# Optimization experiments

Hardware: AMD Instinct MI355X
Metric: run time of the kernel (lower is better)

Reference implementation:

```python
import jax, jax.numpy as jnp
import numpy as np

X_DIM = 512
Y_DIM = 512
HID = 300
N = 2048


def setup_inputs() -> dict:
    key = jax.random.key(0)
    ks = jax.random.split(key, 8)
    scale = 0.05
    return {
        "pos_local": jax.random.normal(ks[0], (N, X_DIM), jnp.float32),
        "pos_global": jax.random.normal(ks[1], (N, Y_DIM), jnp.float32),
        "neg_local": jax.random.normal(ks[2], (N, X_DIM), jnp.float32),
        "neg_global": jax.random.normal(ks[3], (N, Y_DIM), jnp.float32),
        "W1": jax.random.normal(ks[4], (X_DIM + Y_DIM, HID), jnp.float32) * scale,
        "b1": jnp.zeros((HID,), jnp.float32),
        "W2": jax.random.normal(ks[5], (HID, 1), jnp.float32) * scale,
        "b2": jnp.zeros((1,), jnp.float32),
        "batch_size": 256,
    }


def reference(pos_local, pos_global, neg_local, neg_global, W1, b1, W2, b2, batch_size):
    # Split first-layer weight into local/global halves so we never materialize
    # the concatenated pair tensor: F(cat(l, g)) uses l @ W1l + g @ W1g.
    W1l, W1g = W1[:X_DIM], W1[X_DIM:]
    w2, bias2 = W2[:, 0], b2[0]

    # Positive branch: plain batched MLP, chunking does not change the math.
    h0 = jax.nn.relu(pos_local @ W1l + pos_global @ W1g + b1)  # [N, HID]
    t0 = jax.nn.softplus(h0 @ w2 + bias2).mean()

    # Negative branch: per chunk of size B, pair (local_j, global_i),
    # score[i, j] = F(local_j, global_i); logsumexp over j, mean over i.
    nc = neg_local.shape[0] // batch_size
    nl = neg_local.reshape(nc, batch_size, X_DIM)
    ng = neg_global.reshape(nc, batch_size, Y_DIM)

    def chunk_term(carry, lg):
        l, g = lg                                   # [B, x], [B, y]
        lp = l @ W1l                                # [B, HID]
        gp = g @ W1g                                # [B, HID]
        h = jax.nn.relu(gp[:, None, :] + lp[None, :, :] + b1)  # [B, B, HID]
        s = jax.nn.softplus(h @ w2 + bias2)         # [B, B]
        val = jax.scipy.special.logsumexp(s, axis=1).mean()
        return carry + val, None

    total, _ = jax.lax.scan(chunk_term, jnp.float32(0.0), (nl, ng))
    t1 = total / nc

    lower_bound = t0 - t1
    return -lower_bound
```

## Files before the change

kernel.cpp:

```cpp
#include <hip/hip_runtime.h>
#include <math.h>

#define NR   2048
#define XD   512
#define HID  300
#define BS   256
#define NPAD 320
#define KTOT 1024
#define GSTR 304
#define KP   320
#define NNEG 256

typedef __attribute__((ext_vector_type(8))) short bf16x8;
typedef __attribute__((ext_vector_type(4))) float f32x4;

__device__ __forceinline__ float softplus_f(float x) {
    return fmaxf(x, 0.f) + log1pf(__expf(-fabsf(x)));
}
__device__ __forceinline__ unsigned short f2bf(float f) {
    unsigned int u = __float_as_uint(f);
    u += 0x7FFFu + ((u >> 16) & 1u);
    return (unsigned short)(u >> 16);
}

__global__ __launch_bounds__(256) void convert(
    const float* __restrict__ pl, const float* __restrict__ pg,
    const float* __restrict__ nl, const float* __restrict__ ng,
    const float* __restrict__ W1,
    unsigned short* __restrict__ Aneg, unsigned short* __restrict__ Apos,
    unsigned short* __restrict__ Wt, unsigned int* __restrict__ counter)
{
    const int b = blockIdx.x, tid = threadIdx.x;
    if (b == 0 && tid == 0) *counter = 0u;
    if (b < 4096) {
        const int m = (b < 2048) ? b : b - 2048;
        const float* lo = (b < 2048) ? nl : pl;
        const float* hi = (b < 2048) ? ng : pg;
        unsigned short* dst = (b < 2048) ? Aneg : Apos;
        const int kq = tid * 4;
        const float4 v = (kq < XD) ? *(const float4*)(lo + m * XD + kq)
                                   : *(const float4*)(hi + m * XD + kq - XD);
        ushort4 o;
        o.x = f2bf(v.x); o.y = f2bf(v.y); o.z = f2bf(v.z); o.w = f2bf(v.w);
        *(ushort4*)(dst + m * KTOT + kq) = o;
    } else {
        __shared__ unsigned short ts[16][72];
        const int t = b - 4096;
        const int nt = t % 20, kt = t / 20;
        const int n = nt * 16 + (tid & 15);
        const int kl = tid >> 4;
        #pragma unroll
        for (int j = 0; j < 4; ++j) {
            const int k = kt * 64 + kl * 4 + j;
            ts[tid & 15][kl * 4 + j] = f2bf((n < HID) ? W1[k * HID + n] : 0.f);
        }
        __syncthreads();
        const int nw = tid >> 4, kw = (tid & 15) * 4;
        ushort4 o;
        o.x = ts[nw][kw]; o.y = ts[nw][kw + 1]; o.z = ts[nw][kw + 2]; o.w = ts[nw][kw + 3];
        *(ushort4*)(Wt + (nt * 16 + nw) * KTOT + kt * 64 + kw) = o;
    }
}

__global__ __launch_bounds__(64) void mfma_gemm(
    const unsigned short* __restrict__ Aneg, const unsigned short* __restrict__ Apos,
    const unsigned short* __restrict__ Wt, const float* __restrict__ b1,
    float* __restrict__ LP4, float* __restrict__ GPB,
    float* __restrict__ P0a, float* __restrict__ P0b)
{
    const int job = blockIdx.z;
    const int m0 = blockIdx.x * 32, n0 = blockIdx.y * 32;
    const int lane = threadIdx.x;
    const int r = lane & 15, g = lane >> 4;

    const unsigned short* A = (job >= 2) ? Apos : Aneg;
    const int kbeg = (job & 1) ? XD : 0;

    const unsigned short* a0p = A  + (m0 + r) * KTOT + kbeg + 8 * g;
    const unsigned short* a1p = a0p + 16 * KTOT;
    const unsigned short* b0p = Wt + (n0 + r) * KTOT + kbeg + 8 * g;
    const unsigned short* b1p = b0p + 16 * KTOT;

    f32x4 acc00 = {0,0,0,0}, acc01 = {0,0,0,0}, acc10 = {0,0,0,0}, acc11 = {0,0,0,0};

    #pragma unroll
    for (int k = 0; k < XD; k += 32) {
        const bf16x8 a0 = *(const bf16x8*)(a0p + k);
        const bf16x8 a1 = *(const bf16x8*)(a1p + k);
        const bf16x8 w0 = *(const bf16x8*)(b0p + k);
        const bf16x8 w1 = *(const bf16x8*)(b1p + k);
        acc00 = __builtin_amdgcn_mfma_f32_16x16x32_bf16(a0, w0, acc00, 0, 0, 0);
        acc01 = __builtin_amdgcn_mfma_f32_16x16x32_bf16(a0, w1, acc01, 0, 0, 0);
        acc10 = __builtin_amdgcn_mfma_f32_16x16x32_bf16(a1, w0, acc10, 0, 0, 0);
        acc11 = __builtin_amdgcn_mfma_f32_16x16x32_bf16(a1, w1, acc11, 0, 0, 0);
    }

    f32x4 accs[2][2] = {{acc00, acc01}, {acc10, acc11}};
    #pragma unroll
    for (int mi = 0; mi < 2; ++mi) {
        #pragma unroll
        for (int ni = 0; ni < 2; ++ni) {
            const int n = n0 + ni * 16 + r;
            const int mb = m0 + mi * 16 + 4 * g;
            const f32x4 v = accs[mi][ni];
            if (job == 0) {
                float* base = LP4 + ((size_t)(n >> 2) * NR + mb) * 4 + (n & 3);
                base[0] = v[0]; base[4] = v[1]; base[8] = v[2]; base[12] = v[3];
            } else if (n < HID) {
                const float bias = (job == 1) ? b1[n] : 0.f;
                float* out = (job == 1) ? GPB : ((job == 2) ? P0a : P0b);
                #pragma unroll
                for (int j = 0; j < 4; ++j)
                    out[(size_t)(mb + j) * GSTR + n] = v[j] + bias;
            }
        }
    }
}

__global__ __launch_bounds__(512, 2) void negpos(
    const float* __restrict__ LP4, const float* __restrict__ GPB,
    const float* __restrict__ P0a, const float* __restrict__ P0b,
    const float* __restrict__ b1, const float* __restrict__ W2,
    const float* __restrict__ b2,
    float* __restrict__ negE, float* __restrict__ posP,
    unsigned int* __restrict__ counter, float* __restrict__ out)
{
    __shared__ __align__(16) float w2s[KP];
    __shared__ __align__(16) float gbs[8][KP];
    __shared__ __align__(16) float pacc[8][BS][8];
    __shared__ float sC[8];
    __shared__ float red[4][8];
    __shared__ float redp[8];
    __shared__ int sh_last;
    const int tid = threadIdx.x, bid = blockIdx.x;
    const int kh = tid >> 6, lh = tid & 63;
    const float b2v = b2[0];

    const int chunk = bid >> 5, g0 = (bid & 31) * 8;
    const float* gp = GPB + (size_t)(chunk * BS + g0) * GSTR;
    for (int idx = tid; idx < KP; idx += 512) {
        const bool v = idx < HID;
        w2s[idx] = v ? 0.5f * W2[idx] : 0.f;
        #pragma unroll
        for (int g = 0; g < 8; ++g)
            gbs[g][idx] = v ? gp[g * GSTR + idx] : 0.f;
    }
    __syncthreads();

    {
        float c = 0.f;
        #pragma unroll
        for (int h = 0; h < 2; ++h) {
            const int k4 = lh + 64 * h;
            if (k4 < 80) {
                const float4 g4 = *(const float4*)&gbs[kh][k4 * 4];
                const float4 w4 = *(const float4*)&w2s[k4 * 4];
                c += g4.x * w4.x + g4.y * w4.y + g4.z * w4.z + g4.w * w4.w;
            }
        }
        #pragma unroll
        for (int o = 32; o > 0; o >>= 1) c += __shfl_xor(c, o);
        if (lh == 0) sC[kh] = c;
    }

    const int k4beg = 10 * kh;
    const float4* lpb = (const float4*)LP4 + (chunk * BS + lh);

    float acc[8][4];
    float q[4] = {0.f, 0.f, 0.f, 0.f};
    #pragma unroll
    for (int gt = 0; gt < 8; ++gt)
        #pragma unroll
        for (int j = 0; j < 4; ++j) acc[gt][j] = 0.f;

    #pragma unroll
    for (int i = 0; i < 10; ++i) {
        const int k4 = k4beg + i;
        float4 a[4];
        #pragma unroll
        for (int j = 0; j < 4; ++j)
            a[j] = lpb[(size_t)k4 * NR + 64 * j];
        const float4 w4 = *(const float4*)&w2s[k4 * 4];
        #pragma unroll
        for (int j = 0; j < 4; ++j) {
            q[j] = fmaf(w4.x, a[j].x, q[j]);
            q[j] = fmaf(w4.y, a[j].y, q[j]);
            q[j] = fmaf(w4.z, a[j].z, q[j]);
            q[j] = fmaf(w4.w, a[j].w, q[j]);
        }
        #pragma unroll
        for (int gt = 0; gt < 8; ++gt) {
            const float4 g4 = *(const float4*)&gbs[gt][k4 * 4];
            #pragma unroll
            for (int j = 0; j < 4; ++j) {
                acc[gt][j] = fmaf(fabsf(g4.x + a[j].x), w4.x, acc[gt][j]);
                acc[gt][j] = fmaf(fabsf(g4.y + a[j].y), w4.y, acc[gt][j]);
                acc[gt][j] = fmaf(fabsf(g4.z + a[j].z), w4.z, acc[gt][j]);
                acc[gt][j] = fmaf(fabsf(g4.w + a[j].w), w4.w, acc[gt][j]);
            }
        }
    }

    #pragma unroll
    for (int j = 0; j < 4; ++j) {
        *(float4*)&pacc[kh][lh + 64 * j][0] =
            make_float4(acc[0][j] + q[j], acc[1][j] + q[j],
                        acc[2][j] + q[j], acc[3][j] + q[j]);
        *(float4*)&pacc[kh][lh + 64 * j][4] =
            make_float4(acc[4][j] + q[j], acc[5][j] + q[j],
                        acc[6][j] + q[j], acc[7][j] + q[j]);
    }
    __syncthreads();

    if (tid < 256) {
        float s[8];
        #pragma unroll
        for (int gt = 0; gt < 8; ++gt) s[gt] = sC[gt];
        #pragma unroll
        for (int k = 0; k < 8; ++k) {
            const float4 p0 = *(const float4*)&pacc[k][tid][0];
            const float4 p1 = *(const float4*)&pacc[k][tid][4];
            s[0] += p0.x; s[1] += p0.y; s[2] += p0.z; s[3] += p0.w;
            s[4] += p1.x; s[5] += p1.y; s[6] += p1.z; s[7] += p1.w;
        }
        const int wid = tid >> 6;
        #pragma unroll
        for (int gt = 0; gt < 8; ++gt) {
            float v = __expf(softplus_f(s[gt] + b2v));
            #pragma unroll
            for (int o = 32; o > 0; o >>= 1) v += __shfl_xor(v, o);
            if ((tid & 63) == 0) red[wid][gt] = v;
        }
    }
    __syncthreads();
    if (tid == 0) {
        #pragma unroll
        for (int gt = 0; gt < 8; ++gt)
            negE[bid * 8 + gt] = red[0][gt] + red[1][gt] + red[2][gt] + red[3][gt];
    }

    {
        const int row = bid * 8 + kh;
        const float4* ra = (const float4*)(P0a + (size_t)row * GSTR);
        const float4* rb = (const float4*)(P0b + (size_t)row * GSTR);
        float d = 0.f;
        #pragma unroll
        for (int h = 0; h < 2; ++h) {
            const int k4 = lh + 64 * h;
            if (k4 < 75) {
                const float4 aa = ra[k4], bb4 = rb[k4];
                const float4 bb = *(const float4*)(b1 + k4 * 4);
                const float4 wv = *(const float4*)(W2 + k4 * 4);
                d += fmaxf(aa.x + bb4.x + bb.x, 0.f) * wv.x
                   + fmaxf(aa.y + bb4.y + bb.y, 0.f) * wv.y
                   + fmaxf(aa.z + bb4.z + bb.z, 0.f) * wv.z
                   + fmaxf(aa.w + bb4.w + bb.w, 0.f) * wv.w;
            }
        }
        #pragma unroll
        for (int o = 32; o > 0; o >>= 1) d += __shfl_xor(d, o);
        if (lh == 0) redp[kh] = softplus_f(d + b2v);
    }
    __syncthreads();

    if (tid == 0) {
        posP[bid] = redp[0] + redp[1] + redp[2] + redp[3]
                  + redp[4] + redp[5] + redp[6] + redp[7];
        __threadfence();
        const unsigned t = atomicAdd(counter, 1u);
        sh_last = (t == NNEG - 1) ? 1 : 0;
    }
    __syncthreads();
    if (sh_last) {
        __threadfence();
        const volatile float* ne = (const volatile float*)negE;
        const volatile float* pp = (const volatile float*)posP;
        float v = 0.f;
        for (int i = tid; i < 2048; i += 512)
            v += __logf(ne[i]);
        if (tid < NNEG) v -= pp[tid];
        #pragma unroll
        for (int o = 32; o > 0; o >>= 1) v += __shfl_xor(v, o);
        if (lh == 0) redp[kh] = v;
        __syncthreads();
        if (tid == 0)
            out[0] = (redp[0] + redp[1] + redp[2] + redp[3]
                    + redp[4] + redp[5] + redp[6] + redp[7]) * (1.f / 2048.f);
    }
}

extern "C" void kernel_launch(void* const* d_in, const int* in_sizes, int n_in,
                              void* d_out, int out_size, void* d_ws, size_t ws_size,
                              hipStream_t stream)
{
    const float* pl = (const float*)d_in[0];
    const float* pg = (const float*)d_in[1];
    const float* nl = (const float*)d_in[2];
    const float* ng = (const float*)d_in[3];
    const float* W1 = (const float*)d_in[4];
    const float* b1 = (const float*)d_in[5];
    const float* W2 = (const float*)d_in[6];
    const float* b2 = (const float*)d_in[7];

    char* ws = (char*)d_ws;
    unsigned short* Aneg = (unsigned short*)(ws);
    unsigned short* Apos = (unsigned short*)(ws + (4u << 20));
    unsigned short* Wt   = (unsigned short*)(ws + (8u << 20));
    float* LP4  = (float*)(ws + (9u << 20));
    float* GPB  = (float*)(ws + (12u << 20));
    float* P0a  = (float*)(ws + (15u << 20));
    float* P0b  = (float*)(ws + (18u << 20));
    float* negE = (float*)(ws + (21u << 20));
    float* posP = negE + 2048;
    unsigned int* counter = (unsigned int*)(ws + (21u << 20) + 65536);
    float* out  = (float*)d_out;

    hipLaunchKernelGGL(convert, dim3(4096 + 320), dim3(256), 0, stream,
                       pl, pg, nl, ng, W1, Aneg, Apos, Wt, counter);
    hipLaunchKernelGGL(mfma_gemm, dim3(NR / 32, NPAD / 32, 4), dim3(64), 0, stream,
                       Aneg, Apos, Wt, b1, LP4, GPB, P0a, P0b);
    hipLaunchKernelGGL(negpos, dim3(NNEG), dim3(512), 0, stream,
                       LP4, GPB, P0a, P0b, b1, W2, b2, negE, posP, counter, out);
}
```

Measured before the change: 62.31 us.

## Fuse activation bf16 conversion into GEMM and widen negpos blocks to 1024 threads

The standalone conversion of the four activation matrices to bf16 is removed. The GEMM now reads fp32 activations directly and converts them in registers, so the bf16 staging buffers are neither written nor re-read. Only W1 is still pre-converted by a smaller kernel. The pairwise negpos kernel goes from 512 to 1024 threads, splitting the hidden dimension across 16 waves, and runs the positive-branch dot products in parallel with the per-global constant. In exchange it uses twice the shared partial buffer and a launch_bounds(1024,4) register limit that may cause spills, and GEMM tiles re-read fp32 activations at double the byte width.

```diff
diff --git a/kernel.cpp b/kernel.cpp
--- a/kernel.cpp
+++ b/kernel.cpp
@@ -22,48 +22,40 @@
     u += 0x7FFFu + ((u >> 16) & 1u);
     return (unsigned short)(u >> 16);
 }
-
-__global__ __launch_bounds__(256) void convert(
+__device__ __forceinline__ bf16x8 cvt8(const float4 f0, const float4 f1) {
+    bf16x8 r;
+    r[0] = (short)f2bf(f0.x); r[1] = (short)f2bf(f0.y);
+    r[2] = (short)f2bf(f0.z); r[3] = (short)f2bf(f0.w);
+    r[4] = (short)f2bf(f1.x); r[5] = (short)f2bf(f1.y);
+    r[6] = (short)f2bf(f1.z); r[7] = (short)f2bf(f1.w);
+    return r;
+}
+
+__global__ __launch_bounds__(256) void wconvert(
+    const float* __restrict__ W1, unsigned short* __restrict__ Wt,
+    unsigned int* __restrict__ counter)
+{
+    __shared__ unsigned short ts[16][72];
+    const int t = blockIdx.x, tid = threadIdx.x;
+    if (t == 0 && tid == 0) *counter = 0u;
+    const int nt = t % 20, kt = t / 20;
+    const int n = nt * 16 + (tid & 15);
+    const int kl = tid >> 4;
+    #pragma unroll
+    for (int j = 0; j < 4; ++j) {
+        const int k = kt * 64 + kl * 4 + j;
+        ts[tid & 15][kl * 4 + j] = f2bf((n < HID) ? W1[k * HID + n] : 0.f);
+    }
+    __syncthreads();
+    const int nw = tid >> 4, kw = (tid & 15) * 4;
+    ushort4 o;
+    o.x = ts[nw][kw]; o.y = ts[nw][kw + 1]; o.z = ts[nw][kw + 2]; o.w = ts[nw][kw + 3];
+    *(ushort4*)(Wt + (nt * 16 + nw) * KTOT + kt * 64 + kw) = o;
+}
+
+__global__ __launch_bounds__(64) void mfma_gemm(
+    const float* __restrict__ nl, const float* __restrict__ ng,
     const float* __restrict__ pl, const float* __restrict__ pg,
-    const float* __restrict__ nl, const float* __restrict__ ng,
-    const float* __restrict__ W1,
-    unsigned short* __restrict__ Aneg, unsigned short* __restrict__ Apos,
-    unsigned short* __restrict__ Wt, unsigned int* __restrict__ counter)
-{
-    const int b = blockIdx.x, tid = threadIdx.x;
-    if (b == 0 && tid == 0) *counter = 0u;
-    if (b < 4096) {
-        const int m = (b < 2048) ? b : b - 2048;
-        const float* lo = (b < 2048) ? nl : pl;
-        const float* hi = (b < 2048) ? ng : pg;
-        unsigned short* dst = (b < 2048) ? Aneg : Apos;
-        const int kq = tid * 4;
-        const float4 v = (kq < XD) ? *(const float4*)(lo + m * XD + kq)
-                                   : *(const float4*)(hi + m * XD + kq - XD);
-        ushort4 o;
-        o.x = f2bf(v.x); o.y = f2bf(v.y); o.z = f2bf(v.z); o.w = f2bf(v.w);
-        *(ushort4*)(dst + m * KTOT + kq) = o;
-    } else {
-        __shared__ unsigned short ts[16][72];
-        const int t = b - 4096;
-        const int nt = t % 20, kt = t / 20;
-        const int n = nt * 16 + (tid & 15);
-        const int kl = tid >> 4;
-        #pragma unroll
-        for (int j = 0; j < 4; ++j) {
-            const int k = kt * 64 + kl * 4 + j;
-            ts[tid & 15][kl * 4 + j] = f2bf((n < HID) ? W1[k * HID + n] : 0.f);
-        }
-        __syncthreads();
-        const int nw = tid >> 4, kw = (tid & 15) * 4;
-        ushort4 o;
-        o.x = ts[nw][kw]; o.y = ts[nw][kw + 1]; o.z = ts[nw][kw + 2]; o.w = ts[nw][kw + 3];
-        *(ushort4*)(Wt + (nt * 16 + nw) * KTOT + kt * 64 + kw) = o;
-    }
-}
-
-__global__ __launch_bounds__(64) void mfma_gemm(
-    const unsigned short* __restrict__ Aneg, const unsigned short* __restrict__ Apos,
     const unsigned short* __restrict__ Wt, const float* __restrict__ b1,
     float* __restrict__ LP4, float* __restrict__ GPB,
     float* __restrict__ P0a, float* __restrict__ P0b)
@@ -73,20 +65,20 @@
     const int lane = threadIdx.x;
     const int r = lane & 15, g = lane >> 4;
 
-    const unsigned short* A = (job >= 2) ? Apos : Aneg;
-    const int kbeg = (job & 1) ? XD : 0;
-
-    const unsigned short* a0p = A  + (m0 + r) * KTOT + kbeg + 8 * g;
-    const unsigned short* a1p = a0p + 16 * KTOT;
-    const unsigned short* b0p = Wt + (n0 + r) * KTOT + kbeg + 8 * g;
+    const float* Af = (job == 0) ? nl : (job == 1) ? ng : (job == 2) ? pl : pg;
+    const int wb = (job & 1) * XD;
+
+    const float* a0p = Af + (size_t)(m0 + r) * XD + 8 * g;
+    const float* a1p = a0p + 16 * XD;
+    const unsigned short* b0p = Wt + (n0 + r) * KTOT + wb + 8 * g;
     const unsigned short* b1p = b0p + 16 * KTOT;
 
     f32x4 acc00 = {0,0,0,0}, acc01 = {0,0,0,0}, acc10 = {0,0,0,0}, acc11 = {0,0,0,0};
 
     #pragma unroll
     for (int k = 0; k < XD; k += 32) {
-        const bf16x8 a0 = *(const bf16x8*)(a0p + k);
-        const bf16x8 a1 = *(const bf16x8*)(a1p + k);
+        const bf16x8 a0 = cvt8(*(const float4*)(a0p + k), *(const float4*)(a0p + k + 4));
+        const bf16x8 a1 = cvt8(*(const float4*)(a1p + k), *(const float4*)(a1p + k + 4));
         const bf16x8 w0 = *(const bf16x8*)(b0p + k);
         const bf16x8 w1 = *(const bf16x8*)(b1p + k);
         acc00 = __builtin_amdgcn_mfma_f32_16x16x32_bf16(a0, w0, acc00, 0, 0, 0);
@@ -117,7 +109,7 @@
     }
 }
 
-__global__ __launch_bounds__(512, 2) void negpos(
+__global__ __launch_bounds__(1024, 4) void negpos(
     const float* __restrict__ LP4, const float* __restrict__ GPB,
     const float* __restrict__ P0a, const float* __restrict__ P0b,
     const float* __restrict__ b1, const float* __restrict__ W2,
@@ -127,10 +119,11 @@
 {
     __shared__ __align__(16) float w2s[KP];
     __shared__ __align__(16) float gbs[8][KP];
-    __shared__ __align__(16) float pacc[8][BS][8];
+    __shared__ __align__(16) float pacc[16][BS][8];
     __shared__ float sC[8];
     __shared__ float red[4][8];
     __shared__ float redp[8];
+    __shared__ float redf[16];
     __shared__ int sh_last;
     const int tid = threadIdx.x, bid = blockIdx.x;
     const int kh = tid >> 6, lh = tid & 63;
@@ -138,7 +131,7 @@
 
     const int chunk = bid >> 5, g0 = (bid & 31) * 8;
     const float* gp = GPB + (size_t)(chunk * BS + g0) * GSTR;
-    for (int idx = tid; idx < KP; idx += 512) {
+    for (int idx = tid; idx < KP; idx += 1024) {
         const bool v = idx < HID;
         w2s[idx] = v ? 0.5f * W2[idx] : 0.f;
         #pragma unroll
@@ -147,7 +140,7 @@
     }
     __syncthreads();
 
-    {
+    if (kh < 8) {
         float c = 0.f;
         #pragma unroll
         for (int h = 0; h < 2; ++h) {
@@ -161,86 +154,8 @@
         #pragma unroll
         for (int o = 32; o > 0; o >>= 1) c += __shfl_xor(c, o);
         if (lh == 0) sC[kh] = c;
-    }
-
-    const int k4beg = 10 * kh;
-    const float4* lpb = (const float4*)LP4 + (chunk * BS + lh);
-
-    float acc[8][4];
-    float q[4] = {0.f, 0.f, 0.f, 0.f};
-    #pragma unroll
-    for (int gt = 0; gt < 8; ++gt)
-        #pragma unroll
-        for (int j = 0; j < 4; ++j) acc[gt][j] = 0.f;
-
-    #pragma unroll
-    for (int i = 0; i < 10; ++i) {
-        const int k4 = k4beg + i;
-        float4 a[4];
-        #pragma unroll
-        for (int j = 0; j < 4; ++j)
-            a[j] = lpb[(size_t)k4 * NR + 64 * j];
-        const float4 w4 = *(const float4*)&w2s[k4 * 4];
-        #pragma unroll
-        for (int j = 0; j < 4; ++j) {
-            q[j] = fmaf(w4.x, a[j].x, q[j]);
-            q[j] = fmaf(w4.y, a[j].y, q[j]);
-            q[j] = fmaf(w4.z, a[j].z, q[j]);
-            q[j] = fmaf(w4.w, a[j].w, q[j]);
-        }
-        #pragma unroll
-        for (int gt = 0; gt < 8; ++gt) {
-            const float4 g4 = *(const float4*)&gbs[gt][k4 * 4];
-            #pragma unroll
-            for (int j = 0; j < 4; ++j) {
-                acc[gt][j] = fmaf(fabsf(g4.x + a[j].x), w4.x, acc[gt][j]);
-                acc[gt][j] = fmaf(fabsf(g4.y + a[j].y), w4.y, acc[gt][j]);
-                acc[gt][j] = fmaf(fabsf(g4.z + a[j].z), w4.z, acc[gt][j]);
-                acc[gt][j] = fmaf(fabsf(g4.w + a[j].w), w4.w, acc[gt][j]);
-            }
-        }
-    }
-
-    #pragma unroll
-    for (int j = 0; j < 4; ++j) {
-        *(float4*)&pacc[kh][lh + 64 * j][0] =
-            make_float4(acc[0][j] + q[j], acc[1][j] + q[j],
-                        acc[2][j] + q[j], acc[3][j] + q[j]);
-        *(float4*)&pacc[kh][lh + 64 * j][4] =
-            make_float4(acc[4][j] + q[j], acc[5][j] + q[j],
-                        acc[6][j] + q[j], acc[7][j] + q[j]);
-    }
-    __syncthreads();
-
-    if (tid < 256) {
-        float s[8];
-        #pragma unroll
-        for (int gt = 0; gt < 8; ++gt) s[gt] = sC[gt];
-        #pragma unroll
-        for (int k = 0; k < 8; ++k) {
-            const float4 p0 = *(const float4*)&pacc[k][tid][0];
-            const float4 p1 = *(const float4*)&pacc[k][tid][4];
-            s[0] += p0.x; s[1] += p0.y; s[2] += p0.z; s[3] += p0.w;
-            s[4] += p1.x; s[5] += p1.y; s[6] += p1.z; s[7] += p1.w;
-        }
-        const int wid = tid >> 6;
-        #pragma unroll
-        for (int gt = 0; gt < 8; ++gt) {
-            float v = __expf(softplus_f(s[gt] + b2v));
-            #pragma unroll
-            for (int o = 32; o > 0; o >>= 1) v += __shfl_xor(v, o);
-            if ((tid & 63) == 0) red[wid][gt] = v;
-        }
-    }
-    __syncthreads();
-    if (tid == 0) {
-        #pragma unroll
-        for (int gt = 0; gt < 8; ++gt)
-            negE[bid * 8 + gt] = red[0][gt] + red[1][gt] + red[2][gt] + red[3][gt];
-    }
-
-    {
-        const int row = bid * 8 + kh;
+    } else {
+        const int row = bid * 8 + (kh - 8);
         const float4* ra = (const float4*)(P0a + (size_t)row * GSTR);
         const float4* rb = (const float4*)(P0b + (size_t)row * GSTR);
         float d = 0.f;
@@ -259,11 +174,83 @@
         }
         #pragma unroll
         for (int o = 32; o > 0; o >>= 1) d += __shfl_xor(d, o);
-        if (lh == 0) redp[kh] = softplus_f(d + b2v);
-    }
-    __syncthreads();
-
+        if (lh == 0) redp[kh - 8] = softplus_f(d + b2v);
+    }
+
+    const int k4beg = 5 * kh;
+    const float4* lpb = (const float4*)LP4 + (chunk * BS + lh);
+
+    float acc[8][4];
+    float q[4] = {0.f, 0.f, 0.f, 0.f};
+    #pragma unroll
+    for (int gt = 0; gt < 8; ++gt)
+        #pragma unroll
+        for (int j = 0; j < 4; ++j) acc[gt][j] = 0.f;
+
+    #pragma unroll
+    for (int i = 0; i < 5; ++i) {
+        const int k4 = k4beg + i;
+        float4 a[4];
+        #pragma unroll
+        for (int j = 0; j < 4; ++j)
+            a[j] = lpb[(size_t)k4 * NR + 64 * j];
+        const float4 w4 = *(const float4*)&w2s[k4 * 4];
+        #pragma unroll
+        for (int j = 0; j < 4; ++j) {
+            q[j] = fmaf(w4.x, a[j].x, q[j]);
+            q[j] = fmaf(w4.y, a[j].y, q[j]);
+            q[j] = fmaf(w4.z, a[j].z, q[j]);
+            q[j] = fmaf(w4.w, a[j].w, q[j]);
+        }
+        #pragma unroll
+        for (int gt = 0; gt < 8; ++gt) {
+            const float4 g4 = *(const float4*)&gbs[gt][k4 * 4];
+            #pragma unroll
+            for (int j = 0; j < 4; ++j) {
+                acc[gt][j] = fmaf(fabsf(g4.x + a[j].x), w4.x, acc[gt][j]);
+                acc[gt][j] = fmaf(fabsf(g4.y + a[j].y), w4.y, acc[gt][j]);
+                acc[gt][j] = fmaf(fabsf(g4.z + a[j].z), w4.z, acc[gt][j]);
+                acc[gt][j] = fmaf(fabsf(g4.w + a[j].w), w4.w, acc[gt][j]);
+            }
+        }
+    }
+
+    #pragma unroll
+    for (int j = 0; j < 4; ++j) {
+        *(float4*)&pacc[kh][lh + 64 * j][0] =
+            make_float4(acc[0][j] + q[j], acc[1][j] + q[j],
+                        acc[2][j] + q[j], acc[3][j] + q[j]);
+        *(float4*)&pacc[kh][lh + 64 * j][4] =
+            make_float4(acc[4][j] + q[j], acc[5][j] + q[j],
+                        acc[6][j] + q[j], acc[7][j] + q[j]);
+    }
+    __syncthreads();
+
+    if (tid < 256) {
+        float s[8];
+        #pragma unroll
+        for (int gt = 0; gt < 8; ++gt) s[gt] = sC[gt];
+        #pragma unroll
+        for (int k = 0; k < 16; ++k) {
+            const float4 p0 = *(const float4*)&pacc[k][tid][0];
+            const float4 p1 = *(const float4*)&pacc[k][tid][4];
+            s[0] += p0.x; s[1] += p0.y; s[2] += p0.z; s[3] += p0.w;
+            s[4] += p1.x; s[5] += p1.y; s[6] += p1.z; s[7] += p1.w;
+        }
+        const int wid = tid >> 6;
+        #pragma unroll
+        for (int gt = 0; gt < 8; ++gt) {
+            float v = __expf(softplus_f(s[gt] + b2v));
+            #pragma unroll
+            for (int o = 32; o > 0; o >>= 1) v += __shfl_xor(v, o);
+            if ((tid & 63) == 0) red[wid][gt] = v;
+        }
+    }
+    __syncthreads();
     if (tid == 0) {
+        #pragma unroll
+        for (int gt = 0; gt < 8; ++gt)
+            negE[bid * 8 + gt] = red[0][gt] + red[1][gt] + red[2][gt] + red[3][gt];
         posP[bid] = redp[0] + redp[1] + redp[2] + redp[3]
                   + redp[4] + redp[5] + redp[6] + redp[7];
         __threadfence();
@@ -271,21 +258,23 @@
         sh_last = (t == NNEG - 1) ? 1 : 0;
     }
     __syncthreads();
+
     if (sh_last) {
         __threadfence();
         const volatile float* ne = (const volatile float*)negE;
         const volatile float* pp = (const volatile float*)posP;
-        float v = 0.f;
-        for (int i = tid; i < 2048; i += 512)
-            v += __logf(ne[i]);
+        float v = __logf(ne[tid]) + __logf(ne[tid + 1024]);
         if (tid < NNEG) v -= pp[tid];
         #pragma unroll
         for (int o = 32; o > 0; o >>= 1) v += __shfl_xor(v, o);
-        if (lh == 0) redp[kh] = v;
+        if (lh == 0) redf[kh] = v;
         __syncthreads();
-        if (tid == 0)
-            out[0] = (redp[0] + redp[1] + redp[2] + redp[3]
-                    + redp[4] + redp[5] + redp[6] + redp[7]) * (1.f / 2048.f);
+        if (tid == 0) {
+            float s = 0.f;
+            #pragma unroll
+            for (int k = 0; k < 16; ++k) s += redf[k];
+            out[0] = s * (1.f / 2048.f);
+        }
     }
 }
 
@@ -303,22 +292,20 @@
     const float* b2 = (const float*)d_in[7];
 
     char* ws = (char*)d_ws;
-    unsigned short* Aneg = (unsigned short*)(ws);
-    unsigned short* Apos = (unsigned short*)(ws + (4u << 20));
-    unsigned short* Wt   = (unsigned short*)(ws + (8u << 20));
-    float* LP4  = (float*)(ws + (9u << 20));
-    float* GPB  = (float*)(ws + (12u << 20));
-    float* P0a  = (float*)(ws + (15u << 20));
-    float* P0b  = (float*)(ws + (18u << 20));
-    float* negE = (float*)(ws + (21u << 20));
+    unsigned short* Wt = (unsigned short*)(ws);
+    float* LP4  = (float*)(ws + (1u << 20));
+    float* GPB  = (float*)(ws + (5u << 20));
+    float* P0a  = (float*)(ws + (8u << 20));
+    float* P0b  = (float*)(ws + (11u << 20));
+    float* negE = (float*)(ws + (14u << 20));
     float* posP = negE + 2048;
-    unsigned int* counter = (unsigned int*)(ws + (21u << 20) + 65536);
+    unsigned int* counter = (unsigned int*)(ws + (14u << 20) + 65536);
     float* out  = (float*)d_out;
 
-    hipLaunchKernelGGL(convert, dim3(4096 + 320), dim3(256), 0, stream,
-                       pl, pg, nl, ng, W1, Aneg, Apos, Wt, counter);
+    hipLaunchKernelGGL(wconvert, dim3(320), dim3(256), 0, stream,
+                       W1, Wt, counter);
     hipLaunchKernelGGL(mfma_gemm, dim3(NR / 32, NPAD / 32, 4), dim3(64), 0, stream,
-                       Aneg, Apos, Wt, b1, LP4, GPB, P0a, P0b);
-    hipLaunchKernelGGL(negpos, dim3(NNEG), dim3(512), 0, stream,
+                       nl, ng, pl, pg, Wt, b1, LP4, GPB, P0a, P0b);
+    hipLaunchKernelGGL(negpos, dim3(NNEG), dim3(1024), 0, stream,
                        LP4, GPB, P0a, P0b, b1, W2, b2, negE, posP, counter, out);
 }
```

Result: slower. 98.89 us (+58.7%).

## Store LP/GP intermediates in bf16 and stage LP tiles through LDS in two halves

Applied to the files above, without the earlier changes.

The GEMM now writes the local and global projections as bf16 instead of fp32, with the LP buffer packed in groups of eight hidden units. The negative-pair kernel copies each half of the chunk's LP slice into a large shared-memory buffer and converts it back to fp32 on read. The goal is to halve global traffic for the intermediates and replace scattered global loads with LDS reads. In exchange, only four of the eight waves compute during each half, with barriers and a reload in between, which roughly serialises the VALU-heavy pair loop. The bf16 rounding of LP and GP also lowers the accuracy of the scores.

```diff
diff --git a/kernel.cpp b/kernel.cpp
--- a/kernel.cpp
+++ b/kernel.cpp
@@ -8,10 +8,12 @@
 #define NPAD 320
 #define KTOT 1024
 #define GSTR 304
+#define HSTR 304
 #define KP   320
 #define NNEG 256
 
 typedef __attribute__((ext_vector_type(8))) short bf16x8;
+typedef __attribute__((ext_vector_type(8))) unsigned short u16x8;
 typedef __attribute__((ext_vector_type(4))) float f32x4;
 
 __device__ __forceinline__ float softplus_f(float x) {
@@ -21,6 +23,9 @@
     unsigned int u = __float_as_uint(f);
     u += 0x7FFFu + ((u >> 16) & 1u);
     return (unsigned short)(u >> 16);
+}
+__device__ __forceinline__ float bf2f(unsigned short h) {
+    return __uint_as_float((unsigned int)h << 16);
 }
 
 __global__ __launch_bounds__(256) void convert(
@@ -65,7 +70,7 @@
 __global__ __launch_bounds__(64) void mfma_gemm(
     const unsigned short* __restrict__ Aneg, const unsigned short* __restrict__ Apos,
     const unsigned short* __restrict__ Wt, const float* __restrict__ b1,
-    float* __restrict__ LP4, float* __restrict__ GPB,
+    unsigned short* __restrict__ LP4h, unsigned short* __restrict__ GPBh,
     float* __restrict__ P0a, float* __restrict__ P0b)
 {
     const int job = blockIdx.z;
@@ -104,46 +109,69 @@
             const int mb = m0 + mi * 16 + 4 * g;
             const f32x4 v = accs[mi][ni];
             if (job == 0) {
-                float* base = LP4 + ((size_t)(n >> 2) * NR + mb) * 4 + (n & 3);
-                base[0] = v[0]; base[4] = v[1]; base[8] = v[2]; base[12] = v[3];
+                unsigned short* base = LP4h + ((size_t)(n >> 3) * NR + mb) * 8 + (n & 7);
+                base[0]  = f2bf(v[0]); base[8]  = f2bf(v[1]);
+                base[16] = f2bf(v[2]); base[24] = f2bf(v[3]);
             } else if (n < HID) {
-                const float bias = (job == 1) ? b1[n] : 0.f;
-                float* out = (job == 1) ? GPB : ((job == 2) ? P0a : P0b);
-                #pragma unroll
-                for (int j = 0; j < 4; ++j)
-                    out[(size_t)(mb + j) * GSTR + n] = v[j] + bias;
+                if (job == 1) {
+                    const float bias = b1[n];
+                    #pragma unroll
+                    for (int j = 0; j < 4; ++j)
+                        GPBh[(size_t)(mb + j) * HSTR + n] = f2bf(v[j] + bias);
+                } else {
+                    float* out = (job == 2) ? P0a : P0b;
+                    #pragma unroll
+                    for (int j = 0; j < 4; ++j)
+                        out[(size_t)(mb + j) * GSTR + n] = v[j];
+                }
             }
         }
     }
 }
 
 __global__ __launch_bounds__(512, 2) void negpos(
-    const float* __restrict__ LP4, const float* __restrict__ GPB,
+    const unsigned short* __restrict__ LP4h, const unsigned short* __restrict__ GPBh,
     const float* __restrict__ P0a, const float* __restrict__ P0b,
     const float* __restrict__ b1, const float* __restrict__ W2,
     const float* __restrict__ b2,
     float* __restrict__ negE, float* __restrict__ posP,
     unsigned int* __restrict__ counter, float* __restrict__ out)
 {
+    __shared__ __align__(16) unsigned short lps[20][BS][8];
+    __shared__ __align__(16) float gbs[8][KP];
     __shared__ __align__(16) float w2s[KP];
-    __shared__ __align__(16) float gbs[8][KP];
     __shared__ __align__(16) float pacc[8][BS][8];
     __shared__ float sC[8];
     __shared__ float red[4][8];
     __shared__ float redp[8];
     __shared__ int sh_last;
     const int tid = threadIdx.x, bid = blockIdx.x;
-    const int kh = tid >> 6, lh = tid & 63;
+    const int kq = tid >> 6, lh = tid & 63;
     const float b2v = b2[0];
-
     const int chunk = bid >> 5, g0 = (bid & 31) * 8;
-    const float* gp = GPB + (size_t)(chunk * BS + g0) * GSTR;
-    for (int idx = tid; idx < KP; idx += 512) {
-        const bool v = idx < HID;
-        w2s[idx] = v ? 0.5f * W2[idx] : 0.f;
+    const size_t cb = (size_t)chunk * BS;
+
+    const unsigned short* gpb = GPBh + (cb + g0) * HSTR;
+    if (tid < KP) {
+        const bool v = tid < HID;
+        w2s[tid] = v ? 0.5f * W2[tid] : 0.f;
         #pragma unroll
         for (int g = 0; g < 8; ++g)
-            gbs[g][idx] = v ? gp[g * GSTR + idx] : 0.f;
+            gbs[g][tid] = v ? bf2f(gpb[g * HSTR + tid]) : 0.f;
+    }
+
+    {
+        u16x8 tmp[10];
+        #pragma unroll
+        for (int i = 0; i < 10; ++i) {
+            const int f = i * 512 + tid;
+            tmp[i] = *(const u16x8*)(LP4h + ((size_t)(f >> 8) * NR + cb + (f & 255)) * 8);
+        }
+        #pragma unroll
+        for (int i = 0; i < 10; ++i) {
+            const int f = i * 512 + tid;
+            *(u16x8*)&lps[f >> 8][f & 255][0] = tmp[i];
+        }
     }
     __syncthreads();
 
@@ -153,63 +181,88 @@
         for (int h = 0; h < 2; ++h) {
             const int k4 = lh + 64 * h;
             if (k4 < 80) {
-                const float4 g4 = *(const float4*)&gbs[kh][k4 * 4];
+                const float4 g4 = *(const float4*)&gbs[kq][k4 * 4];
                 const float4 w4 = *(const float4*)&w2s[k4 * 4];
                 c += g4.x * w4.x + g4.y * w4.y + g4.z * w4.z + g4.w * w4.w;
             }
         }
         #pragma unroll
         for (int o = 32; o > 0; o >>= 1) c += __shfl_xor(c, o);
-        if (lh == 0) sC[kh] = c;
-    }
-
-    const int k4beg = 10 * kh;
-    const float4* lpb = (const float4*)LP4 + (chunk * BS + lh);
-
-    float acc[8][4];
-    float q[4] = {0.f, 0.f, 0.f, 0.f};
-    #pragma unroll
-    for (int gt = 0; gt < 8; ++gt)
-        #pragma unroll
-        for (int j = 0; j < 4; ++j) acc[gt][j] = 0.f;
-
-    #pragma unroll
-    for (int i = 0; i < 10; ++i) {
-        const int k4 = k4beg + i;
-        float4 a[4];
-        #pragma unroll
-        for (int j = 0; j < 4; ++j)
-            a[j] = lpb[(size_t)k4 * NR + 64 * j];
-        const float4 w4 = *(const float4*)&w2s[k4 * 4];
-        #pragma unroll
-        for (int j = 0; j < 4; ++j) {
-            q[j] = fmaf(w4.x, a[j].x, q[j]);
-            q[j] = fmaf(w4.y, a[j].y, q[j]);
-            q[j] = fmaf(w4.z, a[j].z, q[j]);
-            q[j] = fmaf(w4.w, a[j].w, q[j]);
-        }
-        #pragma unroll
-        for (int gt = 0; gt < 8; ++gt) {
-            const float4 g4 = *(const float4*)&gbs[gt][k4 * 4];
+        if (lh == 0) sC[kq] = c;
+    }
+
+    auto neg_compute = [&](int k8l_off) {
+        float acc[8][4];
+        float q[4] = {0.f, 0.f, 0.f, 0.f};
+        #pragma unroll
+        for (int gt = 0; gt < 8; ++gt)
+            #pragma unroll
+            for (int j = 0; j < 4; ++j) acc[gt][j] = 0.f;
+        const int g8 = 5 * kq;
+        #pragma unroll
+        for (int i = 0; i < 5; ++i) {
+            const int k8g = g8 + i;
+            const int k8l = k8g - k8l_off;
+            const float4 wa = *(const float4*)&w2s[k8g * 8];
+            const float4 wb = *(const float4*)&w2s[k8g * 8 + 4];
+            float fv[4][8];
             #pragma unroll
             for (int j = 0; j < 4; ++j) {
-                acc[gt][j] = fmaf(fabsf(g4.x + a[j].x), w4.x, acc[gt][j]);
-                acc[gt][j] = fmaf(fabsf(g4.y + a[j].y), w4.y, acc[gt][j]);
-                acc[gt][j] = fmaf(fabsf(g4.z + a[j].z), w4.z, acc[gt][j]);
-                acc[gt][j] = fmaf(fabsf(g4.w + a[j].w), w4.w, acc[gt][j]);
-            }
-        }
-    }
-
-    #pragma unroll
-    for (int j = 0; j < 4; ++j) {
-        *(float4*)&pacc[kh][lh + 64 * j][0] =
-            make_float4(acc[0][j] + q[j], acc[1][j] + q[j],
-                        acc[2][j] + q[j], acc[3][j] + q[j]);
-        *(float4*)&pacc[kh][lh + 64 * j][4] =
-            make_float4(acc[4][j] + q[j], acc[5][j] + q[j],
-                        acc[6][j] + q[j], acc[7][j] + q[j]);
-    }
+                const u16x8 hv = *(const u16x8*)&lps[k8l][lh + 64 * j][0];
+                #pragma unroll
+                for (int e = 0; e < 8; ++e) fv[j][e] = bf2f(hv[e]);
+                q[j] = fmaf(wa.x, fv[j][0], q[j]); q[j] = fmaf(wa.y, fv[j][1], q[j]);
+                q[j] = fmaf(wa.z, fv[j][2], q[j]); q[j] = fmaf(wa.w, fv[j][3], q[j]);
+                q[j] = fmaf(wb.x, fv[j][4], q[j]); q[j] = fmaf(wb.y, fv[j][5], q[j]);
+                q[j] = fmaf(wb.z, fv[j][6], q[j]); q[j] = fmaf(wb.w, fv[j][7], q[j]);
+            }
+            #pragma unroll
+            for (int gt = 0; gt < 8; ++gt) {
+                const float4 ga = *(const float4*)&gbs[gt][k8g * 8];
+                const float4 gb = *(const float4*)&gbs[gt][k8g * 8 + 4];
+                #pragma unroll
+                for (int j = 0; j < 4; ++j) {
+                    acc[gt][j] = fmaf(fabsf(ga.x + fv[j][0]), wa.x, acc[gt][j]);
+                    acc[gt][j] = fmaf(fabsf(ga.y + fv[j][1]), wa.y, acc[gt][j]);
+                    acc[gt][j] = fmaf(fabsf(ga.z + fv[j][2]), wa.z, acc[gt][j]);
+                    acc[gt][j] = fmaf(fabsf(ga.w + fv[j][3]), wa.w, acc[gt][j]);
+                    acc[gt][j] = fmaf(fabsf(gb.x + fv[j][4]), wb.x, acc[gt][j]);
+                    acc[gt][j] = fmaf(fabsf(gb.y + fv[j][5]), wb.y, acc[gt][j]);
+                    acc[gt][j] = fmaf(fabsf(gb.z + fv[j][6]), wb.z, acc[gt][j]);
+                    acc[gt][j] = fmaf(fabsf(gb.w + fv[j][7]), wb.w, acc[gt][j]);
+                }
+            }
+        }
+        #pragma unroll
+        for (int j = 0; j < 4; ++j) {
+            *(float4*)&pacc[kq][lh + 64 * j][0] =
+                make_float4(acc[0][j] + q[j], acc[1][j] + q[j],
+                            acc[2][j] + q[j], acc[3][j] + q[j]);
+            *(float4*)&pacc[kq][lh + 64 * j][4] =
+                make_float4(acc[4][j] + q[j], acc[5][j] + q[j],
+                            acc[6][j] + q[j], acc[7][j] + q[j]);
+        }
+    };
+
+    if (kq < 4) neg_compute(0);
+    __syncthreads();
+
+    {
+        u16x8 tmp[10];
+        #pragma unroll
+        for (int i = 0; i < 10; ++i) {
+            const int f = i * 512 + tid;
+            tmp[i] = *(const u16x8*)(LP4h + ((size_t)(20 + (f >> 8)) * NR + cb + (f & 255)) * 8);
+        }
+        #pragma unroll
+        for (int i = 0; i < 10; ++i) {
+            const int f = i * 512 + tid;
+            *(u16x8*)&lps[f >> 8][f & 255][0] = tmp[i];
+        }
+    }
+    __syncthreads();
+
+    if (kq >= 4) neg_compute(20);
     __syncthreads();
 
     if (tid < 256) {
@@ -240,7 +293,7 @@
     }
 
     {
-        const int row = bid * 8 + kh;
+        const int row = bid * 8 + kq;
         const float4* ra = (const float4*)(P0a + (size_t)row * GSTR);
         const float4* rb = (const float4*)(P0b + (size_t)row * GSTR);
         float d = 0.f;
@@ -259,7 +312,7 @@
         }
         #pragma unroll
         for (int o = 32; o > 0; o >>= 1) d += __shfl_xor(d, o);
-        if (lh == 0) redp[kh] = softplus_f(d + b2v);
+        if (lh == 0) redp[kq] = softplus_f(d + b2v);
     }
     __syncthreads();
 
@@ -281,7 +334,7 @@
         if (tid < NNEG) v -= pp[tid];
         #pragma unroll
         for (int o = 32; o > 0; o >>= 1) v += __shfl_xor(v, o);
-        if (lh == 0) redp[kh] = v;
+        if (lh == 0) redp[kq] = v;
         __syncthreads();
         if (tid == 0)
             out[0] = (redp[0] + redp[1] + redp[2] + redp[3]
@@ -306,19 +359,19 @@
     unsigned short* Aneg = (unsigned short*)(ws);
     unsigned short* Apos = (unsigned short*)(ws + (4u << 20));
     unsigned short* Wt   = (unsigned short*)(ws + (8u << 20));
-    float* LP4  = (float*)(ws + (9u << 20));
-    float* GPB  = (float*)(ws + (12u << 20));
-    float* P0a  = (float*)(ws + (15u << 20));
-    float* P0b  = (float*)(ws + (18u << 20));
-    float* negE = (float*)(ws + (21u << 20));
+    unsigned short* LP4h = (unsigned short*)(ws + (9u << 20));
+    unsigned short* GPBh = (unsigned short*)(ws + (11u << 20));
+    float* P0a  = (float*)(ws + (13u << 20));
+    float* P0b  = (float*)(ws + (16u << 20));
+    float* negE = (float*)(ws + (19u << 20));
     float* posP = negE + 2048;
-    unsigned int* counter = (unsigned int*)(ws + (21u << 20) + 65536);
+    unsigned int* counter = (unsigned int*)(ws + (19u << 20) + 65536);
     float* out  = (float*)d_out;
 
     hipLaunchKernelGGL(convert, dim3(4096 + 320), dim3(256), 0, stream,
                        pl, pg, nl, ng, W1, Aneg, Apos, Wt, counter);
     hipLaunchKernelGGL(mfma_gemm, dim3(NR / 32, NPAD / 32, 4), dim3(64), 0, stream,
-                       Aneg, Apos, Wt, b1, LP4, GPB, P0a, P0b);
+                       Aneg, Apos, Wt, b1, LP4h, GPBh, P0a, P0b);
     hipLaunchKernelGGL(negpos, dim3(NNEG), dim3(512), 0, stream,
-                       LP4, GPB, P0a, P0b, b1, W2, b2, negE, posP, counter, out);
-}
+                       LP4h, GPBh, P0a, P0b, b1, W2, b2, negE, posP, counter, out);
+}
```

Result: slower. 70.71 us (+13.5%).
